# Kernel optimization log

Measured on AMD Instinct MI355X. Metric: run time of the kernel, lower is better.

Reference implementation:

```python
import jax, jax.numpy as jnp
import numpy as np

EPS = 1e-5


def setup_inputs() -> dict:
    key = jax.random.key(0)
    ks = jax.random.split(key, 6)
    B, N, F = 8, 8192, 64
    xyzs = jax.random.uniform(ks[0], (B, N, 3), dtype=jnp.float32)
    feats = jax.random.normal(ks[1], (B, N, F), dtype=jnp.float32)
    c_in = 3 + F  # 67
    dims = [(64, c_in), (64, 64), (128, 64)]
    inp = {"xyzs": xyzs, "feats": feats}
    for i, (co, ci) in enumerate(dims, start=1):
        inp[f"w{i}"] = jax.random.normal(ks[1 + i], (co, ci), dtype=jnp.float32) / np.sqrt(ci)
        inp[f"b{i}"] = jnp.zeros((co,), jnp.float32)
        inp[f"g{i}"] = jnp.ones((co,), jnp.float32)
        inp[f"bt{i}"] = jnp.zeros((co,), jnp.float32)
        inp[f"m{i}"] = jnp.zeros((co,), jnp.float32)
        inp[f"v{i}"] = jnp.ones((co,), jnp.float32)
    return inp


def sample_farthest_points(xyz, S):
    # Iterative FPS starting from index 0 (pytorch3d default random_start_point=False).
    B, N, _ = xyz.shape
    barange = jnp.arange(B)

    def step(carry, _):
        mind, last = carry                      # mind: [B,N] min sq-dist to selected set
        lastp = xyz[barange, last]              # [B,3]
        d = jnp.sum((xyz - lastp[:, None, :]) ** 2, -1)
        mind = jnp.minimum(mind, d)
        nxt = jnp.argmax(mind, axis=1).astype(jnp.int32)
        return (mind, nxt), nxt

    init = (jnp.full((B, N), 1e10, xyz.dtype), jnp.zeros((B,), jnp.int32))
    _, rest = jax.lax.scan(step, init, None, length=S - 1)  # [S-1, B]
    idx = jnp.concatenate([jnp.zeros((1, B), jnp.int32), rest], 0).T  # [B,S]
    return xyz[barange[:, None], idx], idx


def ball_query(centers, xyz, K, radius):
    # First-K-in-radius semantics of pytorch3d.ops.ball_query; pad idx with -1,
    # pad gathered points with zeros (masked_gather behavior).
    B, N, _ = xyz.shape
    d2 = (jnp.sum(centers ** 2, -1)[:, :, None]
          + jnp.sum(xyz ** 2, -1)[:, None, :]
          - 2.0 * jnp.einsum('bsd,bnd->bsn', centers, xyz))  # [B,S,N]
    within = d2 <= radius * radius
    skey = jnp.where(within, jnp.arange(N, dtype=jnp.int32), N)
    negvals, idx = jax.lax.top_k(-skey, K)      # K smallest keys = first K in-radius
    valid = (-negvals) < N                       # [B,S,K]
    group_idx = jnp.where(valid, idx, -1)
    gathered = xyz[jnp.arange(B)[:, None, None], jnp.where(valid, idx, 0)]  # [B,S,K,3]
    group_xyz = jnp.where(valid[..., None], gathered, 0.0)
    return group_idx, group_xyz


def _mlp_layer(x, w, b, g, bt, m, v):
    # 1x1 Conv2d over channel axis + BatchNorm (eval stats) + ReLU; x: [B,S,K,Cin]
    y = jnp.einsum('bskc,oc->bsko', x, w) + b
    y = g * (y - m) * jax.lax.rsqrt(v + EPS) + bt
    return jax.nn.relu(y)


def reference(xyzs, feats, w1, b1, g1, bt1, m1, v1,
              w2, b2, g2, bt2, m2, v2, w3, b3, g3, bt3, m3, v3):
    S, K, radius = 2048, 32, 0.2
    B = xyzs.shape[0]
    center_xyzs, _ = sample_farthest_points(xyzs, S)             # [B,S,3]
    group_idxs, group_xyzs = ball_query(center_xyzs, xyzs, K, radius)
    group_xyzs = group_xyzs - center_xyzs[:, :, None, :]          # relative coords
    batch_idxs = jnp.arange(B)[:, None, None]
    gf = feats[batch_idxs, jnp.where(group_idxs < 0, 0, group_idxs)]  # [B,S,K,F]
    gf = jnp.concatenate([group_xyzs, gf], axis=-1)
    gf = gf * (group_idxs != -1)[..., None].astype(gf.dtype)      # zero padded slots
    x = _mlp_layer(gf, w1, b1, g1, bt1, m1, v1)
    x = _mlp_layer(x, w2, b2, g2, bt2, m2, v2)
    x = _mlp_layer(x, w3, b3, g3, bt3, m3, v3)
    center_feats = jnp.max(x, axis=2)                             # max over neighbors
    return center_xyzs, center_feats
```

## Files before the change

kernel.cpp:

```cpp
#include <hip/hip_runtime.h>


#define NPTS 8192
#define SCTR 2048
#define NB   8
#define KNN  32
#define NF   64
#define WT_FLOATS (67*64 + 64*64 + 64*128)
#define RING_U32  (NB * SCTR)

typedef float v2f __attribute__((ext_vector_type(2)));

__device__ __forceinline__ v2f fps_sqdist_v2(v2f px, v2f py, v2f pz,
                                             v2f lx, v2f ly, v2f lz) {
#pragma clang fp contract(off)
  v2f dx = px - lx;
  v2f dy = py - ly;
  v2f dz = pz - lz;
  v2f xx = dx * dx;
  v2f yy = dy * dy;
  v2f zz = dz * dz;
  return (xx + yy) + zz;
}

__device__ __forceinline__ float sumsq3(float x, float y, float z) {
#pragma clang fp contract(off)
  return (x * x + y * y) + z * z;
}

__device__ __forceinline__ float bq_d2(float sc, float sx,
                                       float cx, float cy, float cz,
                                       float x, float y, float z) {
#pragma clang fp contract(off)
  float dt = fmaf(cz, z, fmaf(cy, y, cx * x));
  return (sc + sx) - 2.0f * dt;
}

template <int CTRL>
__device__ __forceinline__ unsigned long long kmax_dpp(unsigned long long k) {
  int lo = (int)(unsigned int)(k & 0xFFFFFFFFull);
  int hi = (int)(unsigned int)(k >> 32);
  int slo = __builtin_amdgcn_update_dpp(lo, lo, CTRL, 0xF, 0xF, false);
  int shi = __builtin_amdgcn_update_dpp(hi, hi, CTRL, 0xF, 0xF, false);
  unsigned long long sk =
      ((unsigned long long)(unsigned int)shi << 32) | (unsigned int)slo;
  return sk > k ? sk : k;
}

__global__ __launch_bounds__(256) void init_kernel(
    const float* __restrict__ w1, const float* __restrict__ w2,
    const float* __restrict__ w3, float* __restrict__ wT,
    unsigned* __restrict__ ring)
{
  const int t = threadIdx.x;
  int idx = blockIdx.x * 256 + t;
  if (idx < RING_U32) ring[idx] = 0u;
  if (idx < 67*64) {
    int c = idx >> 6, o = idx & 63;
    wT[idx] = w1[o*67 + c];
  } else if (idx < 67*64 + 64*64) {
    int r = idx - 67*64; int c = r >> 6, o = r & 63;
    wT[idx] = w2[o*64 + c];
  } else if (idx < 67*64 + 64*64 + 64*128) {
    int r = idx - (67*64 + 64*64); int c = r >> 7, o = r & 127;
    wT[idx] = w3[o*64 + c];
  }
}

__global__ __launch_bounds__(256, 1) void mega_kernel(
    const float* __restrict__ xyzs, const float* __restrict__ feats,
    float* centers, const float* __restrict__ wT, unsigned* ring,
    const float* __restrict__ b1, const float* __restrict__ g1, const float* __restrict__ bt1,
    const float* __restrict__ m1, const float* __restrict__ v1,
    const float* __restrict__ b2, const float* __restrict__ g2, const float* __restrict__ bt2,
    const float* __restrict__ m2, const float* __restrict__ v2,
    const float* __restrict__ b3, const float* __restrict__ g3, const float* __restrict__ bt3,
    const float* __restrict__ m3, const float* __restrict__ v3,
    float* out_feats)
{
  __shared__ __align__(16) float smem[26640];

  if (blockIdx.x < NB) {
    __builtin_amdgcn_s_setprio(3);
    const int b = blockIdx.x;
    const int t = threadIdx.x;
    const float* xb = xyzs + (size_t)b * NPTS * 3;
    unsigned* ring_b = ring + b * SCTR;
    float* cb_ = centers + (size_t)b * SCTR * 3;

    float* sX = smem;
    float* sY = smem + 8192;
    float* sZ = smem + 16384;
    int*  hist = (int*)(smem + 24576);
    unsigned long long* redk = (unsigned long long*)(smem + 26624);

    for (int i = t; i < NPTS; i += 256) {
      sX[i] = xb[3*i+0];
      sY[i] = xb[3*i+1];
      sZ[i] = xb[3*i+2];
    }
    if (t == 0) hist[0] = 0;
    __syncthreads();

    const int t4 = 4 * t;

    const float4 xA = *(const float4*)(sX + 0    + t4);
    const float4 yA = *(const float4*)(sY + 0    + t4);
    const float4 zA = *(const float4*)(sZ + 0    + t4);
    const float4 xB = *(const float4*)(sX + 1024 + t4);
    const float4 yB = *(const float4*)(sY + 1024 + t4);
    const float4 zB = *(const float4*)(sZ + 1024 + t4);
    const float4 xC = *(const float4*)(sX + 2048 + t4);
    const float4 yC = *(const float4*)(sY + 2048 + t4);
    const float4 zC = *(const float4*)(sZ + 2048 + t4);
    const float4 xD = *(const float4*)(sX + 3072 + t4);
    const float4 yD = *(const float4*)(sY + 3072 + t4);
    const float4 zD = *(const float4*)(sZ + 3072 + t4);
    const float4 xE = *(const float4*)(sX + 4096 + t4);
    const float4 yE = *(const float4*)(sY + 4096 + t4);
    const float4 zE = *(const float4*)(sZ + 4096 + t4);
    const float4 xF = *(const float4*)(sX + 5120 + t4);
    const float4 yF = *(const float4*)(sY + 5120 + t4);
    const float4 zF = *(const float4*)(sZ + 5120 + t4);
    const float4 xG = *(const float4*)(sX + 6144 + t4);
    const float4 yG = *(const float4*)(sY + 6144 + t4);
    const float4 zG = *(const float4*)(sZ + 6144 + t4);
    const float4 xH = *(const float4*)(sX + 7168 + t4);
    const float4 yH = *(const float4*)(sY + 7168 + t4);
    const float4 zH = *(const float4*)(sZ + 7168 + t4);

    float4 mA = make_float4(1e10f,1e10f,1e10f,1e10f);
    float4 mB = mA, mC = mA, mD = mA, mE = mA, mF = mA, mG = mA, mH = mA;

    float lx = sX[0], ly = sY[0], lz = sZ[0];
    int stash = 0;

#define FPS_QUAD(QX, QY, QZ, MV, QID, BV, BQ)                                   \
  do {                                                                          \
    v2f d;                                                                      \
    d = fps_sqdist_v2((v2f){QX.x,QX.y}, (v2f){QY.x,QY.y}, (v2f){QZ.x,QZ.y},     \
                      lxv, lyv, lzv);                                           \
    MV.x = fminf(MV.x, d.x);                                                    \
    MV.y = fminf(MV.y, d.y);                                                    \
    d = fps_sqdist_v2((v2f){QX.z,QX.w}, (v2f){QY.z,QY.w}, (v2f){QZ.z,QZ.w},     \
                      lxv, lyv, lzv);                                           \
    MV.z = fminf(MV.z, d.x);                                                    \
    MV.w = fminf(MV.w, d.y);                                                    \
    float qm_ = fmaxf(fmaxf(MV.x, MV.y), fmaxf(MV.z, MV.w));                    \
    if (qm_ > BV) { BV = qm_; BQ = (QID); }                                     \
  } while (0)

    for (int s = 1; s < SCTR; ++s) {
      float bv0 = -1.0f, bv1 = -1.0f; int bq0 = 0, bq1 = 4;
      {
        v2f lxv = {lx, lx}, lyv = {ly, ly}, lzv = {lz, lz};
        FPS_QUAD(xA, yA, zA, mA, 0, bv0, bq0);
        FPS_QUAD(xB, yB, zB, mB, 1, bv0, bq0);
        FPS_QUAD(xC, yC, zC, mC, 2, bv0, bq0);
        FPS_QUAD(xD, yD, zD, mD, 3, bv0, bq0);
        FPS_QUAD(xE, yE, zE, mE, 4, bv1, bq1);
        FPS_QUAD(xF, yF, zF, mF, 5, bv1, bq1);
        FPS_QUAD(xG, yG, zG, mG, 6, bv1, bq1);
        FPS_QUAD(xH, yH, zH, mH, 7, bv1, bq1);
      }
      float bv = bv0; int bq = bq0;
      if (bv1 > bv0) { bv = bv1; bq = bq1; }

      float4 s0_ = (bq & 1) ? mB : mA;
      float4 s1_ = (bq & 1) ? mD : mC;
      float4 s2_ = (bq & 1) ? mF : mE;
      float4 s3_ = (bq & 1) ? mH : mG;
      float4 p0_ = (bq & 2) ? s1_ : s0_;
      float4 p1_ = (bq & 2) ? s3_ : s2_;
      float4 mq_ = (bq & 4) ? p1_ : p0_;
      int j_ = (bv == mq_.x) ? 0 : ((bv == mq_.y) ? 1 : ((bv == mq_.z) ? 2 : 3));
      int bg = (bq << 10) + t4 + j_;

      unsigned long long key =
          ((unsigned long long)__float_as_uint(bv) << 13) |
          (unsigned long long)(8191 - bg);

      key = kmax_dpp<0x111>(key);
      key = kmax_dpp<0x112>(key);
      key = kmax_dpp<0x114>(key);
      key = kmax_dpp<0x118>(key);
      key = kmax_dpp<0x142>(key);
      key = kmax_dpp<0x143>(key);

      int pb = s & 1;
      if ((t & 63) == 63) redk[pb*4 + (t >> 6)] = key;
      __syncthreads();

      unsigned long long k4 = redk[pb*4 + (t & 3)];
      k4 = kmax_dpp<0xB1>(k4);
      k4 = kmax_dpp<0x4E>(k4);

      int i0 = 8191 - (int)(k4 & 0x1FFFull);
      lx = sX[i0]; ly = sY[i0]; lz = sZ[i0];
      if (t == 0) hist[s] = i0;

      if (t < 16 && (s & 15) == t) stash = i0;
      if ((s & 15) == 15 && t < 16) {
        __hip_atomic_store(ring_b + (s - 15) + t,
                           0x80000000u | (unsigned)stash,
                           __ATOMIC_RELAXED, __HIP_MEMORY_SCOPE_AGENT);
      }
    }
#undef FPS_QUAD

    __syncthreads();
    for (int ss = t; ss < SCTR; ss += 256) {
      int i = hist[ss];
      float* o = cb_ + 3 * ss;
      o[0] = sX[i]; o[1] = sY[i]; o[2] = sZ[i];
    }
    return;
  }

  constexpr float R2 = (float)(0.2 * 0.2);
  const int t    = threadIdx.x;
  const int jb   = blockIdx.x - NB;
  const int half = t >> 7;
  const int ht   = t & 127;
  const int w    = ht >> 6;
  const int lane = ht & 63;
  const int cid  = 2 * jb + half;
  const int b    = cid & 7;
  const int s    = cid >> 3;
  const int bid  = b * SCTR + s;
  const float* xb = xyzs + (size_t)b * NPTS * 3;

  float* in_  = smem + half * 4352;
  float* y_   = in_ + 2176;
  int*   gidx = (int*)(smem + 8704) + half * KNN;
  float* csl  = smem + 8768 + half * 4;

  if (ht == 0) {
    int i0 = 0;
    if (s > 0) {
      const unsigned* rp = ring + b * SCTR + s;
      unsigned v;
      while (!((v = __hip_atomic_load(rp, __ATOMIC_RELAXED,
                                      __HIP_MEMORY_SCOPE_AGENT)) & 0x80000000u))
        __builtin_amdgcn_s_sleep(32);
      i0 = (int)(v & 0x1FFFu);
    }
    const float* cg = xb + 3 * i0;
    csl[0] = cg[0]; csl[1] = cg[1]; csl[2] = cg[2];
  }
  __syncthreads();
  const float cx = csl[0], cy = csl[1], cz = csl[2];
  const float sc = sumsq3(cx, cy, cz);

  int cnt = 0;
  for (int base = 0; base < NPTS && cnt < KNN; base += 64) {
    int n = base + lane;
    float x = xb[n*3+0], y = xb[n*3+1], z = xb[n*3+2];
    float sx = sumsq3(x, y, z);
    float d2 = bq_d2(sc, sx, cx, cy, cz, x, y, z);
    bool within = (d2 <= R2);
    unsigned long long mk = __ballot(within);
    int rank = __popcll(mk & ((1ull << lane) - 1ull));
    int slot = cnt + rank;
    if (within && slot < KNN) gidx[slot] = n;
    cnt += (int)__popcll(mk);
  }
  if (cnt > KNN) cnt = KNN;
  __syncthreads();

#pragma unroll 4
  for (int k2 = 0; k2 < 16; ++k2) {
    int k = 2*k2 + w;
    int gk = (k < cnt) ? gidx[k] : -1;
    float fv = 0.f, xv = 0.f;
    if (gk >= 0) {
      fv = feats[((size_t)b * NPTS + gk) * NF + lane];
      if (lane < 3) xv = xb[gk*3 + lane] - csl[lane];
    }
    in_[k*68 + 3 + lane] = fv;
    if (lane < 3) in_[k*68 + lane] = xv;
    if (lane == 3) in_[k*68 + 67] = 0.f;
  }
  __syncthreads();

  const int g  = lane >> 3;
  const int h  = lane & 7;
  const int ob = w*32 + 4*h;
  const float* w1T = wT;
  const float* w2T = wT + 67*64;
  const float* w3T = wT + 67*64 + 64*64;

#define FMA_COL(AS0, AS1, AS2, AS3, WV)                                      \
  do {                                                                       \
    acc[0][0]=fmaf(AS0, WV.x, acc[0][0]); acc[0][1]=fmaf(AS0, WV.y, acc[0][1]); \
    acc[0][2]=fmaf(AS0, WV.z, acc[0][2]); acc[0][3]=fmaf(AS0, WV.w, acc[0][3]); \
    acc[1][0]=fmaf(AS1, WV.x, acc[1][0]); acc[1][1]=fmaf(AS1, WV.y, acc[1][1]); \
    acc[1][2]=fmaf(AS1, WV.z, acc[1][2]); acc[1][3]=fmaf(AS1, WV.w, acc[1][3]); \
    acc[2][0]=fmaf(AS2, WV.x, acc[2][0]); acc[2][1]=fmaf(AS2, WV.y, acc[2][1]); \
    acc[2][2]=fmaf(AS2, WV.z, acc[2][2]); acc[2][3]=fmaf(AS2, WV.w, acc[2][3]); \
    acc[3][0]=fmaf(AS3, WV.x, acc[3][0]); acc[3][1]=fmaf(AS3, WV.y, acc[3][1]); \
    acc[3][2]=fmaf(AS3, WV.z, acc[3][2]); acc[3][3]=fmaf(AS3, WV.w, acc[3][3]); \
  } while (0)

#define MLP_CHUNK(SRC, WBASE, WSTRIDE, WOFF)                                 \
  do {                                                                       \
    float4 a0 = *(const float4*)((SRC) + (4*g+0)*68 + c0);                   \
    float4 a1 = *(const float4*)((SRC) + (4*g+1)*68 + c0);                   \
    float4 a2 = *(const float4*)((SRC) + (4*g+2)*68 + c0);                   \
    float4 a3 = *(const float4*)((SRC) + (4*g+3)*68 + c0);                   \
    float4 wv0 = *(const float4*)(WBASE + (c0+0)*(WSTRIDE) + (WOFF));        \
    float4 wv1 = *(const float4*)(WBASE + (c0+1)*(WSTRIDE) + (WOFF));        \
    float4 wv2 = *(const float4*)(WBASE + (c0+2)*(WSTRIDE) + (WOFF));        \
    float4 wv3 = *(const float4*)(WBASE + (c0+3)*(WSTRIDE) + (WOFF));        \
    FMA_COL(a0.x, a1.x, a2.x, a3.x, wv0);                                    \
    FMA_COL(a0.y, a1.y, a2.y, a3.y, wv1);                                    \
    FMA_COL(a0.z, a1.z, a2.z, a3.z, wv2);                                    \
    FMA_COL(a0.w, a1.w, a2.w, a3.w, wv3);                                    \
  } while (0)

  {
    float acc[4][4];
#pragma unroll
    for (int i=0;i<4;++i)
#pragma unroll
      for (int j=0;j<4;++j) acc[i][j]=0.f;
#pragma unroll 2
    for (int c0 = 0; c0 < 68; c0 += 4) {
      MLP_CHUNK(in_, w1T, 64, ob);
    }
    float scl[4], shf[4];
#pragma unroll
    for (int j=0;j<4;++j) {
      int o = ob + j;
      float r = g1[o] * rsqrtf(v1[o] + 1e-5f);
      scl[j] = r;
      shf[j] = (b1[o] - m1[o]) * r + bt1[o];
    }
#pragma unroll
    for (int i=0;i<4;++i) {
      float4 out;
      out.x = fmaxf(fmaf(acc[i][0], scl[0], shf[0]), 0.f);
      out.y = fmaxf(fmaf(acc[i][1], scl[1], shf[1]), 0.f);
      out.z = fmaxf(fmaf(acc[i][2], scl[2], shf[2]), 0.f);
      out.w = fmaxf(fmaf(acc[i][3], scl[3], shf[3]), 0.f);
      *(float4*)(y_ + (4*g+i)*68 + ob) = out;
    }
  }
  __syncthreads();

  {
    float acc[4][4];
#pragma unroll
    for (int i=0;i<4;++i)
#pragma unroll
      for (int j=0;j<4;++j) acc[i][j]=0.f;
#pragma unroll 2
    for (int c0 = 0; c0 < 64; c0 += 4) {
      MLP_CHUNK(y_, w2T, 64, ob);
    }
    float scl[4], shf[4];
#pragma unroll
    for (int j=0;j<4;++j) {
      int o = ob + j;
      float r = g2[o] * rsqrtf(v2[o] + 1e-5f);
      scl[j] = r;
      shf[j] = (b2[o] - m2[o]) * r + bt2[o];
    }
    __syncthreads();
#pragma unroll
    for (int i=0;i<4;++i) {
      float4 out;
      out.x = fmaxf(fmaf(acc[i][0], scl[0], shf[0]), 0.f);
      out.y = fmaxf(fmaf(acc[i][1], scl[1], shf[1]), 0.f);
      out.z = fmaxf(fmaf(acc[i][2], scl[2], shf[2]), 0.f);
      out.w = fmaxf(fmaf(acc[i][3], scl[3], shf[3]), 0.f);
      *(float4*)(in_ + (4*g+i)*68 + ob) = out;
    }
  }
  __syncthreads();

  for (int p = 0; p < 2; ++p) {
    const int o3 = w*64 + p*32 + 4*h;
    float acc[4][4];
#pragma unroll
    for (int i=0;i<4;++i)
#pragma unroll
      for (int j=0;j<4;++j) acc[i][j]=0.f;
#pragma unroll 2
    for (int c0 = 0; c0 < 64; c0 += 4) {
      MLP_CHUNK(in_, w3T, 128, o3);
    }
    float scl[4], shf[4];
#pragma unroll
    for (int j=0;j<4;++j) {
      int o = o3 + j;
      float r = g3[o] * rsqrtf(v3[o] + 1e-5f);
      scl[j] = r;
      shf[j] = (b3[o] - m3[o]) * r + bt3[o];
    }
    float vm[4];
#pragma unroll
    for (int j=0;j<4;++j) {
      float q0 = fmaxf(fmaf(acc[0][j], scl[j], shf[j]), 0.f);
      float q1 = fmaxf(fmaf(acc[1][j], scl[j], shf[j]), 0.f);
      float q2 = fmaxf(fmaf(acc[2][j], scl[j], shf[j]), 0.f);
      float q3 = fmaxf(fmaf(acc[3][j], scl[j], shf[j]), 0.f);
      vm[j] = fmaxf(fmaxf(q0,q1), fmaxf(q2,q3));
    }
#pragma unroll
    for (int mk = 8; mk < 64; mk <<= 1) {
#pragma unroll
      for (int j=0;j<4;++j) vm[j] = fmaxf(vm[j], __shfl_xor(vm[j], mk));
    }
    if (g == 0) {
      float* dst = out_feats + (size_t)bid*128 + o3;
      *(float4*)dst = make_float4(vm[0], vm[1], vm[2], vm[3]);
    }
  }
#undef MLP_CHUNK
#undef FMA_COL
}

extern "C" void kernel_launch(void* const* d_in, const int* in_sizes, int n_in,
                              void* d_out, int out_size, void* d_ws, size_t ws_size,
                              hipStream_t stream) {
  const float* xyzs  = (const float*)d_in[0];
  const float* feats = (const float*)d_in[1];
  const float* w1  = (const float*)d_in[2];
  const float* b1  = (const float*)d_in[3];
  const float* g1  = (const float*)d_in[4];
  const float* bt1 = (const float*)d_in[5];
  const float* m1  = (const float*)d_in[6];
  const float* v1  = (const float*)d_in[7];
  const float* w2  = (const float*)d_in[8];
  const float* b2  = (const float*)d_in[9];
  const float* g2  = (const float*)d_in[10];
  const float* bt2 = (const float*)d_in[11];
  const float* m2  = (const float*)d_in[12];
  const float* v2  = (const float*)d_in[13];
  const float* w3  = (const float*)d_in[14];
  const float* b3  = (const float*)d_in[15];
  const float* g3  = (const float*)d_in[16];
  const float* bt3 = (const float*)d_in[17];
  const float* m3  = (const float*)d_in[18];
  const float* v3  = (const float*)d_in[19];

  float* out       = (float*)d_out;
  float* centers   = out;
  float* out_feats = out + (size_t)NB * SCTR * 3;
  float* wT        = (float*)d_ws;
  unsigned* ring   = (unsigned*)((float*)d_ws + WT_FLOATS);

  hipLaunchKernelGGL(init_kernel, dim3(65), dim3(256), 0, stream,
                     w1, w2, w3, wT, ring);
  hipLaunchKernelGGL(mega_kernel, dim3(NB + NB * SCTR / 2), dim3(256), 0, stream,
                     xyzs, feats, centers, wT, ring,
                     b1, g1, bt1, m1, v1,
                     b2, g2, bt2, m2, v2,
                     b3, g3, bt3, m3, v3,
                     out_feats);
}
```

Before: 1.916 ms.

## Run two FPS chains per block and drop shared-memory point staging

Each FPS block now handles two batches at once, interleaving their independent distance and argmax chains so one barrier per step serves both chains. The block count for FPS falls from 8 to 4. Points are loaded straight from global memory into registers with a de-interleaving float4 load. The per-step coordinate lookup now reads global memory (cached) instead of LDS, which shrinks shared memory from about 104 KB to about 35 KB so consumer blocks can reach higher occupancy. The risks are roughly double the per-thread work on the serial FPS critical path, higher register pressure from holding two point sets, and global-load latency for each selected point.

```diff
diff --git a/kernel.cpp b/kernel.cpp
--- a/kernel.cpp
+++ b/kernel.cpp
@@ -4,6 +4,7 @@
 #define NPTS 8192
 #define SCTR 2048
 #define NB   8
+#define NFPS 4
 #define KNN  32
 #define NF   64
 #define WT_FLOATS (67*64 + 64*64 + 64*128)
@@ -78,62 +79,52 @@
     const float* __restrict__ m3, const float* __restrict__ v3,
     float* out_feats)
 {
-  __shared__ __align__(16) float smem[26640];
-
-  if (blockIdx.x < NB) {
+  __shared__ __align__(16) float smem[8784];
+
+  if (blockIdx.x < NFPS) {
     __builtin_amdgcn_s_setprio(3);
-    const int b = blockIdx.x;
+    const int bi = blockIdx.x;
     const int t = threadIdx.x;
-    const float* xb = xyzs + (size_t)b * NPTS * 3;
-    unsigned* ring_b = ring + b * SCTR;
-    float* cb_ = centers + (size_t)b * SCTR * 3;
-
-    float* sX = smem;
-    float* sY = smem + 8192;
-    float* sZ = smem + 16384;
-    int*  hist = (int*)(smem + 24576);
-    unsigned long long* redk = (unsigned long long*)(smem + 26624);
-
-    for (int i = t; i < NPTS; i += 256) {
-      sX[i] = xb[3*i+0];
-      sY[i] = xb[3*i+1];
-      sZ[i] = xb[3*i+2];
-    }
-    if (t == 0) hist[0] = 0;
-    __syncthreads();
-
     const int t4 = 4 * t;
-
-    const float4 xA = *(const float4*)(sX + 0    + t4);
-    const float4 yA = *(const float4*)(sY + 0    + t4);
-    const float4 zA = *(const float4*)(sZ + 0    + t4);
-    const float4 xB = *(const float4*)(sX + 1024 + t4);
-    const float4 yB = *(const float4*)(sY + 1024 + t4);
-    const float4 zB = *(const float4*)(sZ + 1024 + t4);
-    const float4 xC = *(const float4*)(sX + 2048 + t4);
-    const float4 yC = *(const float4*)(sY + 2048 + t4);
-    const float4 zC = *(const float4*)(sZ + 2048 + t4);
-    const float4 xD = *(const float4*)(sX + 3072 + t4);
-    const float4 yD = *(const float4*)(sY + 3072 + t4);
-    const float4 zD = *(const float4*)(sZ + 3072 + t4);
-    const float4 xE = *(const float4*)(sX + 4096 + t4);
-    const float4 yE = *(const float4*)(sY + 4096 + t4);
-    const float4 zE = *(const float4*)(sZ + 4096 + t4);
-    const float4 xF = *(const float4*)(sX + 5120 + t4);
-    const float4 yF = *(const float4*)(sY + 5120 + t4);
-    const float4 zF = *(const float4*)(sZ + 5120 + t4);
-    const float4 xG = *(const float4*)(sX + 6144 + t4);
-    const float4 yG = *(const float4*)(sY + 6144 + t4);
-    const float4 zG = *(const float4*)(sZ + 6144 + t4);
-    const float4 xH = *(const float4*)(sX + 7168 + t4);
-    const float4 yH = *(const float4*)(sY + 7168 + t4);
-    const float4 zH = *(const float4*)(sZ + 7168 + t4);
-
-    float4 mA = make_float4(1e10f,1e10f,1e10f,1e10f);
-    float4 mB = mA, mC = mA, mD = mA, mE = mA, mF = mA, mG = mA, mH = mA;
-
-    float lx = sX[0], ly = sY[0], lz = sZ[0];
-    int stash = 0;
+    const float* xb0 = xyzs + (size_t)(2*bi)     * NPTS * 3;
+    const float* xb1 = xyzs + (size_t)(2*bi + 1) * NPTS * 3;
+    unsigned* ring0 = ring + (2*bi)     * SCTR;
+    unsigned* ring1 = ring + (2*bi + 1) * SCTR;
+    float* cb0 = centers + (size_t)(2*bi)     * SCTR * 3;
+    float* cb1 = centers + (size_t)(2*bi + 1) * SCTR * 3;
+    int* hist0 = (int*)smem;
+    int* hist1 = (int*)smem + 2048;
+    unsigned long long* redk = (unsigned long long*)(smem + 4096);
+
+#define LOADQ(QX, QY, QZ, XB, QOFF)                                           \
+    { const float4* p_ = (const float4*)((XB) + (size_t)3 * ((QOFF) + t4));   \
+      float4 l0 = p_[0], l1 = p_[1], l2 = p_[2];                              \
+      QX = make_float4(l0.x, l0.w, l1.z, l2.y);                               \
+      QY = make_float4(l0.y, l1.x, l1.w, l2.z);                               \
+      QZ = make_float4(l0.z, l1.y, l2.x, l2.w); }
+
+    float4 xA0,yA0,zA0,xB0,yB0,zB0,xC0,yC0,zC0,xD0,yD0,zD0;
+    float4 xE0,yE0,zE0,xF0,yF0,zF0,xG0,yG0,zG0,xH0,yH0,zH0;
+    float4 xA1,yA1,zA1,xB1,yB1,zB1,xC1,yC1,zC1,xD1,yD1,zD1;
+    float4 xE1,yE1,zE1,xF1,yF1,zF1,xG1,yG1,zG1,xH1,yH1,zH1;
+    LOADQ(xA0,yA0,zA0, xb0, 0);    LOADQ(xB0,yB0,zB0, xb0, 1024);
+    LOADQ(xC0,yC0,zC0, xb0, 2048); LOADQ(xD0,yD0,zD0, xb0, 3072);
+    LOADQ(xE0,yE0,zE0, xb0, 4096); LOADQ(xF0,yF0,zF0, xb0, 5120);
+    LOADQ(xG0,yG0,zG0, xb0, 6144); LOADQ(xH0,yH0,zH0, xb0, 7168);
+    LOADQ(xA1,yA1,zA1, xb1, 0);    LOADQ(xB1,yB1,zB1, xb1, 1024);
+    LOADQ(xC1,yC1,zC1, xb1, 2048); LOADQ(xD1,yD1,zD1, xb1, 3072);
+    LOADQ(xE1,yE1,zE1, xb1, 4096); LOADQ(xF1,yF1,zF1, xb1, 5120);
+    LOADQ(xG1,yG1,zG1, xb1, 6144); LOADQ(xH1,yH1,zH1, xb1, 7168);
+#undef LOADQ
+
+    float4 mA0 = make_float4(1e10f,1e10f,1e10f,1e10f);
+    float4 mB0=mA0,mC0=mA0,mD0=mA0,mE0=mA0,mF0=mA0,mG0=mA0,mH0=mA0;
+    float4 mA1=mA0,mB1=mA0,mC1=mA0,mD1=mA0,mE1=mA0,mF1=mA0,mG1=mA0,mH1=mA0;
+
+    if (t == 0) { hist0[0] = 0; hist1[0] = 0; }
+    float lx0 = xb0[0], ly0 = xb0[1], lz0 = xb0[2];
+    float lx1 = xb1[0], ly1 = xb1[1], lz1 = xb1[2];
+    int stash0 = 0, stash1 = 0;
 
 #define FPS_QUAD(QX, QY, QZ, MV, QID, BV, BQ)                                   \
   do {                                                                          \
@@ -150,76 +141,98 @@
     if (qm_ > BV) { BV = qm_; BQ = (QID); }                                     \
   } while (0)
 
+#define CHAIN_LOCAL(SUF, CH, LX, LY, LZ)                                        \
+    {                                                                           \
+      float bv0 = -1.0f, bv1 = -1.0f; int bq0 = 0, bq1 = 4;                     \
+      {                                                                         \
+        v2f lxv = {LX, LX}, lyv = {LY, LY}, lzv = {LZ, LZ};                     \
+        FPS_QUAD(xA##SUF, yA##SUF, zA##SUF, mA##SUF, 0, bv0, bq0);              \
+        FPS_QUAD(xB##SUF, yB##SUF, zB##SUF, mB##SUF, 1, bv0, bq0);              \
+        FPS_QUAD(xC##SUF, yC##SUF, zC##SUF, mC##SUF, 2, bv0, bq0);              \
+        FPS_QUAD(xD##SUF, yD##SUF, zD##SUF, mD##SUF, 3, bv0, bq0);              \
+        FPS_QUAD(xE##SUF, yE##SUF, zE##SUF, mE##SUF, 4, bv1, bq1);              \
+        FPS_QUAD(xF##SUF, yF##SUF, zF##SUF, mF##SUF, 5, bv1, bq1);              \
+        FPS_QUAD(xG##SUF, yG##SUF, zG##SUF, mG##SUF, 6, bv1, bq1);              \
+        FPS_QUAD(xH##SUF, yH##SUF, zH##SUF, mH##SUF, 7, bv1, bq1);              \
+      }                                                                         \
+      float bv = bv0; int bq = bq0;                                             \
+      if (bv1 > bv0) { bv = bv1; bq = bq1; }                                    \
+      float4 s0_ = (bq & 1) ? mB##SUF : mA##SUF;                                \
+      float4 s1_ = (bq & 1) ? mD##SUF : mC##SUF;                                \
+      float4 s2_ = (bq & 1) ? mF##SUF : mE##SUF;                                \
+      float4 s3_ = (bq & 1) ? mH##SUF : mG##SUF;                                \
+      float4 p0_ = (bq & 2) ? s1_ : s0_;                                        \
+      float4 p1_ = (bq & 2) ? s3_ : s2_;                                        \
+      float4 mq_ = (bq & 4) ? p1_ : p0_;                                        \
+      int j_ = (bv == mq_.x) ? 0 : ((bv == mq_.y) ? 1 : ((bv == mq_.z) ? 2 : 3)); \
+      int bg = (bq << 10) + t4 + j_;                                            \
+      unsigned long long key =                                                  \
+          ((unsigned long long)__float_as_uint(bv) << 13) |                     \
+          (unsigned long long)(8191 - bg);                                      \
+      key = kmax_dpp<0x111>(key);                                               \
+      key = kmax_dpp<0x112>(key);                                               \
+      key = kmax_dpp<0x114>(key);                                               \
+      key = kmax_dpp<0x118>(key);                                               \
+      key = kmax_dpp<0x142>(key);                                               \
+      key = kmax_dpp<0x143>(key);                                               \
+      if ((t & 63) == 63) redk[(CH)*8 + pb*4 + (t >> 6)] = key;                 \
+    }
+
     for (int s = 1; s < SCTR; ++s) {
-      float bv0 = -1.0f, bv1 = -1.0f; int bq0 = 0, bq1 = 4;
-      {
-        v2f lxv = {lx, lx}, lyv = {ly, ly}, lzv = {lz, lz};
-        FPS_QUAD(xA, yA, zA, mA, 0, bv0, bq0);
-        FPS_QUAD(xB, yB, zB, mB, 1, bv0, bq0);
-        FPS_QUAD(xC, yC, zC, mC, 2, bv0, bq0);
-        FPS_QUAD(xD, yD, zD, mD, 3, bv0, bq0);
-        FPS_QUAD(xE, yE, zE, mE, 4, bv1, bq1);
-        FPS_QUAD(xF, yF, zF, mF, 5, bv1, bq1);
-        FPS_QUAD(xG, yG, zG, mG, 6, bv1, bq1);
-        FPS_QUAD(xH, yH, zH, mH, 7, bv1, bq1);
+      const int pb = s & 1;
+      CHAIN_LOCAL(0, 0, lx0, ly0, lz0)
+      CHAIN_LOCAL(1, 1, lx1, ly1, lz1)
+      __syncthreads();
+
+      unsigned long long k40 = redk[pb*4 + (t & 3)];
+      k40 = kmax_dpp<0xB1>(k40);
+      k40 = kmax_dpp<0x4E>(k40);
+      int i00 = 8191 - (int)(k40 & 0x1FFFull);
+      unsigned long long k41 = redk[8 + pb*4 + (t & 3)];
+      k41 = kmax_dpp<0xB1>(k41);
+      k41 = kmax_dpp<0x4E>(k41);
+      int i01 = 8191 - (int)(k41 & 0x1FFFull);
+
+      const float* wp0 = xb0 + 3 * i00;
+      const float* wp1 = xb1 + 3 * i01;
+      lx0 = wp0[0]; ly0 = wp0[1]; lz0 = wp0[2];
+      lx1 = wp1[0]; ly1 = wp1[1]; lz1 = wp1[2];
+      if (t == 0) { hist0[s] = i00; hist1[s] = i01; }
+
+      if (t < 16 && (s & 15) == t) stash0 = i00;
+      if (t >= 16 && t < 32 && (s & 15) == (t - 16)) stash1 = i01;
+      if ((s & 15) == 15) {
+        if (t < 16) {
+          __hip_atomic_store(ring0 + (s - 15) + t,
+                             0x80000000u | (unsigned)stash0,
+                             __ATOMIC_RELAXED, __HIP_MEMORY_SCOPE_AGENT);
+        } else if (t < 32) {
+          __hip_atomic_store(ring1 + (s - 15) + (t - 16),
+                             0x80000000u | (unsigned)stash1,
+                             __ATOMIC_RELAXED, __HIP_MEMORY_SCOPE_AGENT);
+        }
       }
-      float bv = bv0; int bq = bq0;
-      if (bv1 > bv0) { bv = bv1; bq = bq1; }
-
-      float4 s0_ = (bq & 1) ? mB : mA;
-      float4 s1_ = (bq & 1) ? mD : mC;
-      float4 s2_ = (bq & 1) ? mF : mE;
-      float4 s3_ = (bq & 1) ? mH : mG;
-      float4 p0_ = (bq & 2) ? s1_ : s0_;
-      float4 p1_ = (bq & 2) ? s3_ : s2_;
-      float4 mq_ = (bq & 4) ? p1_ : p0_;
-      int j_ = (bv == mq_.x) ? 0 : ((bv == mq_.y) ? 1 : ((bv == mq_.z) ? 2 : 3));
-      int bg = (bq << 10) + t4 + j_;
-
-      unsigned long long key =
-          ((unsigned long long)__float_as_uint(bv) << 13) |
-          (unsigned long long)(8191 - bg);
-
-      key = kmax_dpp<0x111>(key);
-      key = kmax_dpp<0x112>(key);
-      key = kmax_dpp<0x114>(key);
-      key = kmax_dpp<0x118>(key);
-      key = kmax_dpp<0x142>(key);
-      key = kmax_dpp<0x143>(key);
-
-      int pb = s & 1;
-      if ((t & 63) == 63) redk[pb*4 + (t >> 6)] = key;
-      __syncthreads();
-
-      unsigned long long k4 = redk[pb*4 + (t & 3)];
-      k4 = kmax_dpp<0xB1>(k4);
-      k4 = kmax_dpp<0x4E>(k4);
-
-      int i0 = 8191 - (int)(k4 & 0x1FFFull);
-      lx = sX[i0]; ly = sY[i0]; lz = sZ[i0];
-      if (t == 0) hist[s] = i0;
-
-      if (t < 16 && (s & 15) == t) stash = i0;
-      if ((s & 15) == 15 && t < 16) {
-        __hip_atomic_store(ring_b + (s - 15) + t,
-                           0x80000000u | (unsigned)stash,
-                           __ATOMIC_RELAXED, __HIP_MEMORY_SCOPE_AGENT);
-      }
-    }
+    }
+#undef CHAIN_LOCAL
 #undef FPS_QUAD
 
     __syncthreads();
     for (int ss = t; ss < SCTR; ss += 256) {
-      int i = hist[ss];
-      float* o = cb_ + 3 * ss;
-      o[0] = sX[i]; o[1] = sY[i]; o[2] = sZ[i];
+      int i = hist0[ss];
+      const float* p = xb0 + 3 * i;
+      float* o = cb0 + 3 * ss;
+      o[0] = p[0]; o[1] = p[1]; o[2] = p[2];
+      i = hist1[ss];
+      p = xb1 + 3 * i;
+      o = cb1 + 3 * ss;
+      o[0] = p[0]; o[1] = p[1]; o[2] = p[2];
     }
     return;
   }
 
   constexpr float R2 = (float)(0.2 * 0.2);
   const int t    = threadIdx.x;
-  const int jb   = blockIdx.x - NB;
+  const int jb   = blockIdx.x - NFPS;
   const int half = t >> 7;
   const int ht   = t & 127;
   const int w    = ht >> 6;
@@ -453,7 +466,7 @@
 
   hipLaunchKernelGGL(init_kernel, dim3(65), dim3(256), 0, stream,
                      w1, w2, w3, wT, ring);
-  hipLaunchKernelGGL(mega_kernel, dim3(NB + NB * SCTR / 2), dim3(256), 0, stream,
+  hipLaunchKernelGGL(mega_kernel, dim3(NFPS + NB * SCTR / 2), dim3(256), 0, stream,
                      xyzs, feats, centers, wT, ring,
                      b1, g1, bt1, m1, v1,
                      b2, g2, bt2, m2, v2,
```

After: 3.431 ms. 79.1% more time.

## Pack two FPS batches per 512-thread block and read FPS points from global

Applied to the files above, without the earlier changes.

The mega kernel now uses 512-thread blocks. Each farthest-point-sampling block handles two batches, one per 256-thread half, so only four such blocks are launched. Each grouping/MLP block now processes four centers instead of two. FPS no longer stages xyz into shared memory: coordinates are read as float4 from global into registers, and the selected point is fetched from global on every iteration. This cuts LDS use and the block count, but it puts a global load on the serial FPS critical path. A single barrier now couples the two batches. The new launch bound may also limit registers for the register-heavy FPS loop.

```diff
diff --git a/kernel.cpp b/kernel.cpp
--- a/kernel.cpp
+++ b/kernel.cpp
@@ -4,6 +4,7 @@
 #define NPTS 8192
 #define SCTR 2048
 #define NB   8
+#define NFPS 4
 #define KNN  32
 #define NF   64
 #define WT_FLOATS (67*64 + 64*64 + 64*128)
@@ -67,7 +68,7 @@
   }
 }
 
-__global__ __launch_bounds__(256, 1) void mega_kernel(
+__global__ __launch_bounds__(512, 2) void mega_kernel(
     const float* __restrict__ xyzs, const float* __restrict__ feats,
     float* centers, const float* __restrict__ wT, unsigned* ring,
     const float* __restrict__ b1, const float* __restrict__ g1, const float* __restrict__ bt1,
@@ -78,61 +79,43 @@
     const float* __restrict__ m3, const float* __restrict__ v3,
     float* out_feats)
 {
-  __shared__ __align__(16) float smem[26640];
-
-  if (blockIdx.x < NB) {
+  __shared__ __align__(16) float smem[17552];
+
+  if (blockIdx.x < NFPS) {
     __builtin_amdgcn_s_setprio(3);
-    const int b = blockIdx.x;
-    const int t = threadIdx.x;
+    const int bi = blockIdx.x;
+    const int t  = threadIdx.x;
+    const int ch = t >> 8;
+    const int tc = t & 255;
+    const int t4 = 4 * tc;
+    const int b  = 2*bi + ch;
     const float* xb = xyzs + (size_t)b * NPTS * 3;
     unsigned* ring_b = ring + b * SCTR;
     float* cb_ = centers + (size_t)b * SCTR * 3;
-
-    float* sX = smem;
-    float* sY = smem + 8192;
-    float* sZ = smem + 16384;
-    int*  hist = (int*)(smem + 24576);
-    unsigned long long* redk = (unsigned long long*)(smem + 26624);
-
-    for (int i = t; i < NPTS; i += 256) {
-      sX[i] = xb[3*i+0];
-      sY[i] = xb[3*i+1];
-      sZ[i] = xb[3*i+2];
-    }
-    if (t == 0) hist[0] = 0;
-    __syncthreads();
-
-    const int t4 = 4 * t;
-
-    const float4 xA = *(const float4*)(sX + 0    + t4);
-    const float4 yA = *(const float4*)(sY + 0    + t4);
-    const float4 zA = *(const float4*)(sZ + 0    + t4);
-    const float4 xB = *(const float4*)(sX + 1024 + t4);
-    const float4 yB = *(const float4*)(sY + 1024 + t4);
-    const float4 zB = *(const float4*)(sZ + 1024 + t4);
-    const float4 xC = *(const float4*)(sX + 2048 + t4);
-    const float4 yC = *(const float4*)(sY + 2048 + t4);
-    const float4 zC = *(const float4*)(sZ + 2048 + t4);
-    const float4 xD = *(const float4*)(sX + 3072 + t4);
-    const float4 yD = *(const float4*)(sY + 3072 + t4);
-    const float4 zD = *(const float4*)(sZ + 3072 + t4);
-    const float4 xE = *(const float4*)(sX + 4096 + t4);
-    const float4 yE = *(const float4*)(sY + 4096 + t4);
-    const float4 zE = *(const float4*)(sZ + 4096 + t4);
-    const float4 xF = *(const float4*)(sX + 5120 + t4);
-    const float4 yF = *(const float4*)(sY + 5120 + t4);
-    const float4 zF = *(const float4*)(sZ + 5120 + t4);
-    const float4 xG = *(const float4*)(sX + 6144 + t4);
-    const float4 yG = *(const float4*)(sY + 6144 + t4);
-    const float4 zG = *(const float4*)(sZ + 6144 + t4);
-    const float4 xH = *(const float4*)(sX + 7168 + t4);
-    const float4 yH = *(const float4*)(sY + 7168 + t4);
-    const float4 zH = *(const float4*)(sZ + 7168 + t4);
+    int* hist = (int*)smem + ch * 2048;
+    unsigned long long* redk =
+        (unsigned long long*)(smem + 4096) + ch * 8;
+
+#define LOADQ(QX, QY, QZ, QOFF)                                               \
+    { const float4* p_ = (const float4*)(xb + (size_t)3 * ((QOFF) + t4));     \
+      float4 l0 = p_[0], l1 = p_[1], l2 = p_[2];                              \
+      QX = make_float4(l0.x, l0.w, l1.z, l2.y);                               \
+      QY = make_float4(l0.y, l1.x, l1.w, l2.z);                               \
+      QZ = make_float4(l0.z, l1.y, l2.x, l2.w); }
+
+    float4 xA, yA, zA, xB, yB, zB, xC, yC, zC, xD, yD, zD;
+    float4 xE, yE, zE, xF, yF, zF, xG, yG, zG, xH, yH, zH;
+    LOADQ(xA, yA, zA, 0);    LOADQ(xB, yB, zB, 1024);
+    LOADQ(xC, yC, zC, 2048); LOADQ(xD, yD, zD, 3072);
+    LOADQ(xE, yE, zE, 4096); LOADQ(xF, yF, zF, 5120);
+    LOADQ(xG, yG, zG, 6144); LOADQ(xH, yH, zH, 7168);
+#undef LOADQ
 
     float4 mA = make_float4(1e10f,1e10f,1e10f,1e10f);
     float4 mB = mA, mC = mA, mD = mA, mE = mA, mF = mA, mG = mA, mH = mA;
 
-    float lx = sX[0], ly = sY[0], lz = sZ[0];
+    if (tc == 0) hist[0] = 0;
+    float lx = xb[0], ly = xb[1], lz = xb[2];
     int stash = 0;
 
 #define FPS_QUAD(QX, QY, QZ, MV, QID, BV, BQ)                                   \
@@ -151,6 +134,7 @@
   } while (0)
 
     for (int s = 1; s < SCTR; ++s) {
+      const int pb = s & 1;
       float bv0 = -1.0f, bv1 = -1.0f; int bq0 = 0, bq1 = 4;
       {
         v2f lxv = {lx, lx}, lyv = {ly, ly}, lzv = {lz, lz};
@@ -187,21 +171,21 @@
       key = kmax_dpp<0x142>(key);
       key = kmax_dpp<0x143>(key);
 
-      int pb = s & 1;
-      if ((t & 63) == 63) redk[pb*4 + (t >> 6)] = key;
+      if ((tc & 63) == 63) redk[pb*4 + (tc >> 6)] = key;
       __syncthreads();
 
-      unsigned long long k4 = redk[pb*4 + (t & 3)];
+      unsigned long long k4 = redk[pb*4 + (tc & 3)];
       k4 = kmax_dpp<0xB1>(k4);
       k4 = kmax_dpp<0x4E>(k4);
 
       int i0 = 8191 - (int)(k4 & 0x1FFFull);
-      lx = sX[i0]; ly = sY[i0]; lz = sZ[i0];
-      if (t == 0) hist[s] = i0;
-
-      if (t < 16 && (s & 15) == t) stash = i0;
-      if ((s & 15) == 15 && t < 16) {
-        __hip_atomic_store(ring_b + (s - 15) + t,
+      const float* wp = xb + 3 * i0;
+      lx = wp[0]; ly = wp[1]; lz = wp[2];
+      if (tc == 0) hist[s] = i0;
+
+      if (tc < 16 && (s & 15) == tc) stash = i0;
+      if ((s & 15) == 15 && tc < 16) {
+        __hip_atomic_store(ring_b + (s - 15) + tc,
                            0x80000000u | (unsigned)stash,
                            __ATOMIC_RELAXED, __HIP_MEMORY_SCOPE_AGENT);
       }
@@ -209,22 +193,23 @@
 #undef FPS_QUAD
 
     __syncthreads();
-    for (int ss = t; ss < SCTR; ss += 256) {
+    for (int ss = tc; ss < SCTR; ss += 256) {
       int i = hist[ss];
+      const float* p = xb + 3 * i;
       float* o = cb_ + 3 * ss;
-      o[0] = sX[i]; o[1] = sY[i]; o[2] = sZ[i];
+      o[0] = p[0]; o[1] = p[1]; o[2] = p[2];
     }
     return;
   }
 
   constexpr float R2 = (float)(0.2 * 0.2);
   const int t    = threadIdx.x;
-  const int jb   = blockIdx.x - NB;
+  const int jb   = blockIdx.x - NFPS;
   const int half = t >> 7;
   const int ht   = t & 127;
   const int w    = ht >> 6;
   const int lane = ht & 63;
-  const int cid  = 2 * jb + half;
+  const int cid  = 4 * jb + half;
   const int b    = cid & 7;
   const int s    = cid >> 3;
   const int bid  = b * SCTR + s;
@@ -232,8 +217,8 @@
 
   float* in_  = smem + half * 4352;
   float* y_   = in_ + 2176;
-  int*   gidx = (int*)(smem + 8704) + half * KNN;
-  float* csl  = smem + 8768 + half * 4;
+  int*   gidx = (int*)(smem + 17408) + half * KNN;
+  float* csl  = smem + 17536 + half * 4;
 
   if (ht == 0) {
     int i0 = 0;
@@ -453,7 +438,7 @@
 
   hipLaunchKernelGGL(init_kernel, dim3(65), dim3(256), 0, stream,
                      w1, w2, w3, wT, ring);
-  hipLaunchKernelGGL(mega_kernel, dim3(NB + NB * SCTR / 2), dim3(256), 0, stream,
+  hipLaunchKernelGGL(mega_kernel, dim3(NFPS + NB * SCTR / 4), dim3(512), 0, stream,
                      xyzs, feats, centers, wT, ring,
                      b1, g1, bt1, m1, v1,
                      b2, g2, bt2, m2, v2,
```

Measured after the change: 3.095 ms. +61.5%, slower.
